# Kernel optimization log

Hardware: AMD Instinct MI355X
Metric: run time of the kernel (lower is better)

Reference implementation:

```python
import jax, jax.numpy as jnp
import numpy as np

N_NODES = 100000


def gcn_conv(x, edge_index, W, b):
    """PyG-style GCNConv: symmetric-normalized A+I propagation of x @ W, plus bias."""
    n = x.shape[0]
    src, dst = edge_index[0], edge_index[1]
    loops = jnp.arange(n, dtype=src.dtype)
    src = jnp.concatenate([src, loops])  # add self loops
    dst = jnp.concatenate([dst, loops])
    deg = jax.ops.segment_sum(jnp.ones_like(src, dtype=x.dtype), dst, num_segments=n)
    dinv = jnp.where(deg > 0, jax.lax.rsqrt(deg), 0.0)
    norm = dinv[src] * dinv[dst]  # [E+n]
    h = x @ W  # [n, out]
    msg = h[src] * norm[:, None]  # gather + scale
    out = jax.ops.segment_sum(msg, dst, num_segments=n)  # scatter-add
    return out + b


def setup_inputs() -> dict:
    key = jax.random.key(0)
    ks = jax.random.split(key, 5)
    x = jax.random.normal(ks[0], (N_NODES, 4), dtype=jnp.float32)
    edge_index = jax.random.randint(ks[1], (2, 3200000), 0, N_NODES, dtype=jnp.int64)
    W1 = jax.random.normal(ks[2], (4, 64), dtype=jnp.float32) * 0.5
    b1 = jnp.zeros((64,), dtype=jnp.float32)
    W2 = jax.random.normal(ks[3], (64, 32), dtype=jnp.float32) * 0.125
    b2 = jnp.zeros((32,), dtype=jnp.float32)
    return {"x": x, "edge_index": edge_index, "W1": W1, "b1": b1, "W2": W2, "b2": b2}


def reference(x, edge_index, W1, b1, W2, b2):
    h = gcn_conv(x, edge_index, W1, b1)
    h = jax.nn.relu(h)
    # F.dropout with training=False is identity (eval-mode reference)
    h = gcn_conv(h, edge_index, W2, b2)
    return jnp.mean(h, axis=0)  # [32]
```

## Files before the change

kernel.cpp:

```cpp
#include <hip/hip_runtime.h>

#define ST 512
#define EPB 8192
#define CT 1024
#define FT 1024
#define S_LOG 8
#define S 256
#define CAP 8912
#define MAXB 512

__device__ __forceinline__ void gAtomAdd(float* p, float v) {
    unsafeAtomicAdd(p, v);
}

__global__ void k_init(int* __restrict__ cur_d, int* __restrict__ cur_s,
                       float* __restrict__ g, int nb) {
    int t = threadIdx.x;
    if (t < nb) { cur_d[t] = t * CAP; cur_s[t] = t * CAP; }
    if (t < 64) g[t] = 0.0f;
}

__global__ void __launch_bounds__(ST) k_sctr2(
        const int4* __restrict__ src4, const int4* __restrict__ dst4, int E,
        int* __restrict__ cur_d, int* __restrict__ cur_s,
        unsigned* __restrict__ rec_d, unsigned* __restrict__ rec_s, int nb) {
    __shared__ unsigned lrec[EPB];
    __shared__ unsigned short lbkt[EPB];
    __shared__ int cnt[MAXB];
    __shared__ int lst[MAXB];
    __shared__ int gb[MAXB];
    int t = threadIdx.x;
    int E4 = E >> 2;
    int b4 = blockIdx.x * (EPB / 4);
    int m = min(EPB, E - blockIdx.x * EPB);

    int4 dk[4], sk[4];
    bool v[4];
    #pragma unroll
    for (int k = 0; k < 4; ++k) {
        int idx = b4 + k * ST + t;
        v[k] = idx < E4;
        if (v[k]) { dk[k] = dst4[idx]; sk[k] = src4[idx]; }
    }

    for (int ph = 0; ph < 2; ++ph) {
        int* cursor = ph ? cur_s : cur_d;
        unsigned* rec = ph ? rec_s : rec_d;
        cnt[t] = 0;
        __syncthreads();
        int rk[16];
        #pragma unroll
        for (int k = 0; k < 4; ++k) {
            if (v[k]) {
                int4 K = ph ? sk[k] : dk[k];
                rk[4 * k + 0] = atomicAdd(&cnt[K.x >> S_LOG], 1);
                rk[4 * k + 1] = atomicAdd(&cnt[K.y >> S_LOG], 1);
                rk[4 * k + 2] = atomicAdd(&cnt[K.z >> S_LOG], 1);
                rk[4 * k + 3] = atomicAdd(&cnt[K.w >> S_LOG], 1);
            }
        }
        __syncthreads();
        int c = cnt[t];
        for (int o = 1; o < MAXB; o <<= 1) {
            int u = (t >= o) ? cnt[t - o] : 0;
            __syncthreads();
            cnt[t] += u;
            __syncthreads();
        }
        lst[t] = cnt[t] - c;
        gb[t] = (c > 0) ? atomicAdd(&cursor[t], c) : 0;
        __syncthreads();
        #pragma unroll
        for (int k = 0; k < 4; ++k) {
            if (v[k]) {
                int4 K = ph ? sk[k] : dk[k];
                int4 P = ph ? dk[k] : sk[k];
                int bb, p;
                bb = K.x >> S_LOG; p = lst[bb] + rk[4 * k + 0];
                lrec[p] = ((unsigned)P.x << S_LOG) | (unsigned)(K.x & (S - 1));
                lbkt[p] = (unsigned short)bb;
                bb = K.y >> S_LOG; p = lst[bb] + rk[4 * k + 1];
                lrec[p] = ((unsigned)P.y << S_LOG) | (unsigned)(K.y & (S - 1));
                lbkt[p] = (unsigned short)bb;
                bb = K.z >> S_LOG; p = lst[bb] + rk[4 * k + 2];
                lrec[p] = ((unsigned)P.z << S_LOG) | (unsigned)(K.z & (S - 1));
                lbkt[p] = (unsigned short)bb;
                bb = K.w >> S_LOG; p = lst[bb] + rk[4 * k + 3];
                lrec[p] = ((unsigned)P.w << S_LOG) | (unsigned)(K.w & (S - 1));
                lbkt[p] = (unsigned short)bb;
            }
        }
        __syncthreads();
        for (int i = t; i < m; i += ST) {
            int bb = lbkt[i];
            rec[gb[bb] + (i - lst[bb])] = lrec[i];
        }
        __syncthreads();
    }
}

__global__ void __launch_bounds__(CT) k_csry(
        unsigned* __restrict__ rec, const int* __restrict__ cur_d,
        const float4* __restrict__ x, float* __restrict__ dinv,
        float4* __restrict__ y, int* __restrict__ nst_g, int* __restrict__ nend_g,
        int n) {
    __shared__ unsigned lrec[CAP];
    __shared__ int cnt[S];
    __shared__ int nst[S];
    int b = blockIdx.x, t = threadIdx.x;
    int lo = b * CAP;
    int m = cur_d[b] - lo;
    if (t < S) cnt[t] = 0;
    __syncthreads();
    unsigned rv[9]; int rr[9];
    #pragma unroll
    for (int k = 0; k < 9; ++k) {
        int i = t + k * CT;
        if (i < m) {
            unsigned r = rec[lo + i];
            rv[k] = r;
            rr[k] = atomicAdd(&cnt[r & (S - 1)], 1);
        }
    }
    __syncthreads();
    int deg = (t < S) ? cnt[t] : 0;
    int nd = (b << S_LOG) + t;
    if (t < S && nd < n) {
        float dv = rsqrtf((float)deg + 1.0f);
        dinv[nd] = dv;
        float4 xi = x[nd];
        y[nd] = make_float4(dv * xi.x, dv * xi.y, dv * xi.z, dv * xi.w);
    }
    for (int o = 1; o < S; o <<= 1) {
        int u = (t < S && t >= o) ? cnt[t - o] : 0;
        __syncthreads();
        if (t < S) cnt[t] += u;
        __syncthreads();
    }
    if (t < S) {
        int st = cnt[t] - deg;
        nst[t] = st;
        if (nd < n) { nst_g[nd] = lo + st; nend_g[nd] = lo + st + deg; }
    }
    __syncthreads();
    #pragma unroll
    for (int k = 0; k < 9; ++k) {
        int i = t + k * CT;
        if (i < m) lrec[nst[rv[k] & (S - 1)] + rr[k]] = rv[k] >> S_LOG;
    }
    __syncthreads();
    for (int i = t; i < m; i += CT) rec[lo + i] = lrec[i];
}

__global__ void __launch_bounds__(FT) k_fuse(
        const unsigned* __restrict__ rec_d, const unsigned* __restrict__ rec_s,
        const int* __restrict__ cur_s, const int* __restrict__ nst_g,
        const int* __restrict__ nend_g, const float4* __restrict__ y,
        const float* __restrict__ dinv,
        const float* __restrict__ W1, const float* __restrict__ b1,
        float* __restrict__ g, int n) {
    __shared__ float a[S];
    __shared__ float4 lp1[S];
    __shared__ float red[FT];
    int b = blockIdx.x, t = threadIdx.x;
    if (t < S) a[t] = 0.0f;
    __syncthreads();
    int lo = b * CAP;
    int m = cur_s[b] - lo;
    int m4 = m >> 2;
    const uint4* rec4 = (const uint4*)(rec_s + lo);
    for (int i = t; i < m4; i += FT) {
        uint4 r = rec4[i];
        float d0 = dinv[r.x >> S_LOG], d1 = dinv[r.y >> S_LOG];
        float d2 = dinv[r.z >> S_LOG], d3 = dinv[r.w >> S_LOG];
        atomicAdd(&a[r.x & (S - 1)], d0);
        atomicAdd(&a[r.y & (S - 1)], d1);
        atomicAdd(&a[r.z & (S - 1)], d2);
        atomicAdd(&a[r.w & (S - 1)], d3);
    }
    for (int i = (m4 << 2) + t; i < m; i += FT) {
        unsigned r = rec_s[lo + i];
        atomicAdd(&a[r & (S - 1)], dinv[r >> S_LOG]);
    }
    int node = t >> 2, q = t & 3;
    int nd = (b << S_LOG) + node;
    if (nd < n) {
        int j1 = nend_g[nd];
        int j = nst_g[nd] + q;
        float a0 = 0.0f, a1 = 0.0f, a2 = 0.0f, a3 = 0.0f;
        for (; j + 12 < j1; j += 16) {
            int s0 = rec_d[j], s1 = rec_d[j + 4], s2 = rec_d[j + 8], s3 = rec_d[j + 12];
            float4 y0 = y[s0], y1 = y[s1], y2 = y[s2], y3 = y[s3];
            a0 += y0.x + y1.x + y2.x + y3.x;
            a1 += y0.y + y1.y + y2.y + y3.y;
            a2 += y0.z + y1.z + y2.z + y3.z;
            a3 += y0.w + y1.w + y2.w + y3.w;
        }
        for (; j < j1; j += 4) {
            float4 ys = y[rec_d[j]];
            a0 += ys.x; a1 += ys.y; a2 += ys.z; a3 += ys.w;
        }
        a0 += __shfl_down(a0, 2); a1 += __shfl_down(a1, 2);
        a2 += __shfl_down(a2, 2); a3 += __shfl_down(a3, 2);
        a0 += __shfl_down(a0, 1); a1 += __shfl_down(a1, 1);
        a2 += __shfl_down(a2, 1); a3 += __shfl_down(a3, 1);
        if (q == 0) {
            float di = dinv[nd];
            lp1[node] = make_float4(di * a0, di * a1, di * a2, di * a3);
        }
    }
    __syncthreads();
    int c = t & 63, w = t >> 6;
    float w0 = W1[c], w1 = W1[64 + c], w2 = W1[128 + c], w3 = W1[192 + c];
    float bb = b1[c];
    int nb0 = b << S_LOG;
    float facc = 0.0f;
    for (int k = w; k < S; k += 16) {
        int ndk = nb0 + k;
        if (ndk >= n) break;
        float di = dinv[ndk];
        float4 p = lp1[k];
        float4 yi = y[ndk];
        float h0 = fmaf(di, yi.x, p.x);
        float h1 = fmaf(di, yi.y, p.y);
        float h2 = fmaf(di, yi.z, p.z);
        float h3 = fmaf(di, yi.w, p.w);
        float h = fmaf(h0, w0, fmaf(h1, w1, fmaf(h2, w2, fmaf(h3, w3, bb))));
        h = fmaxf(h, 0.0f);
        float wi = fmaf(di, a[k], di * di);
        facc = fmaf(wi, h, facc);
    }
    red[t] = facc;
    __syncthreads();
    if (t < 64) {
        float s = red[t];
        #pragma unroll
        for (int o = 1; o < 16; ++o) s += red[t + 64 * o];
        gAtomAdd(&g[t], s);
    }
}

__global__ void k_final(const float* __restrict__ g, const float* __restrict__ W2,
                        const float* __restrict__ b2, float* __restrict__ out, float inv_n) {
    int j = threadIdx.x;
    if (j < 32) {
        float a = 0.0f;
        #pragma unroll
        for (int c = 0; c < 64; ++c) a = fmaf(g[c], W2[c * 32 + j], a);
        out[j] = fmaf(a, inv_n, b2[j]);
    }
}

extern "C" void kernel_launch(void* const* d_in, const int* in_sizes, int n_in,
                              void* d_out, int out_size, void* d_ws, size_t ws_size,
                              hipStream_t stream) {
    const float* x  = (const float*)d_in[0];
    const int*   ei = (const int*)d_in[1];
    const float* W1 = (const float*)d_in[2];
    const float* b1 = (const float*)d_in[3];
    const float* W2 = (const float*)d_in[4];
    const float* b2 = (const float*)d_in[5];
    float* out = (float*)d_out;

    int n = in_sizes[0] / 4;
    int E = in_sizes[1] / 2;
    const int* src = ei;
    const int* dst = ei + E;
    int NB = (n + S - 1) >> S_LOG;

    char* ws = (char*)d_ws;
    int* cur_d = (int*)ws;
    int* cur_s = cur_d + 512;
    float* g   = (float*)(cur_s + 512);
    size_t ctrl = 1600;
    unsigned* rec_d = (unsigned*)ws + ctrl;
    unsigned* rec_s = rec_d + (size_t)NB * CAP;
    float* y    = (float*)(rec_s + (size_t)NB * CAP);
    float* dinv = y + 4 * (size_t)n;
    int* nst_g  = (int*)(dinv + (size_t)n);
    int* nend_g = nst_g + (size_t)n;

    int NSB = (E + EPB - 1) / EPB;

    k_init<<<1, 512, 0, stream>>>(cur_d, cur_s, g, NB);
    k_sctr2<<<NSB, ST, 0, stream>>>((const int4*)src, (const int4*)dst, E,
                                    cur_d, cur_s, rec_d, rec_s, NB);
    k_csry<<<NB, CT, 0, stream>>>(rec_d, cur_d, (const float4*)x, dinv,
                                  (float4*)y, nst_g, nend_g, n);
    k_fuse<<<NB, FT, 0, stream>>>(rec_d, rec_s, cur_s, nst_g, nend_g,
                                  (const float4*)y, dinv, W1, b1, g, n);
    k_final<<<1, 64, 0, stream>>>(g, W2, b2, out, 1.0f / (float)n);
}
```

Measured before the change: 154.5 us.

## Replace per-bucket CSR sort with LDS atomic scatter-add aggregation

The in-bucket counting sort that built CSR rows (prefix scan, LDS reorder, rec_d write-back, nst/nend arrays) is removed. Degrees are now counted with LDS atomics, and the first-layer aggregation scatter-adds gathered y rows into four per-component LDS arrays instead of walking sorted CSR rows. This cuts a pass over the records and the scan/sync overhead. The cost is about four times more LDS float atomics, possible contention on hot nodes, and a nondeterministic summation order. Block sizes drop from 1024 to 512 threads.

```diff
diff --git a/kernel.cpp b/kernel.cpp
--- a/kernel.cpp
+++ b/kernel.cpp
@@ -2,8 +2,8 @@
 
 #define ST 512
 #define EPB 8192
-#define CT 1024
-#define FT 1024
+#define DT 512
+#define FT 512
 #define S_LOG 8
 #define S 256
 #define CAP 8912
@@ -99,114 +99,94 @@
     }
 }
 
-__global__ void __launch_bounds__(CT) k_csry(
-        unsigned* __restrict__ rec, const int* __restrict__ cur_d,
+__global__ void __launch_bounds__(DT) k_dy(
+        const unsigned* __restrict__ rec_d, const int* __restrict__ cur_d,
         const float4* __restrict__ x, float* __restrict__ dinv,
-        float4* __restrict__ y, int* __restrict__ nst_g, int* __restrict__ nend_g,
-        int n) {
-    __shared__ unsigned lrec[CAP];
+        float4* __restrict__ y, int n) {
     __shared__ int cnt[S];
-    __shared__ int nst[S];
     int b = blockIdx.x, t = threadIdx.x;
     int lo = b * CAP;
-    int m = cur_d[b] - lo;
+    int md = cur_d[b] - lo;
     if (t < S) cnt[t] = 0;
     __syncthreads();
-    unsigned rv[9]; int rr[9];
-    #pragma unroll
-    for (int k = 0; k < 9; ++k) {
-        int i = t + k * CT;
-        if (i < m) {
-            unsigned r = rec[lo + i];
-            rv[k] = r;
-            rr[k] = atomicAdd(&cnt[r & (S - 1)], 1);
-        }
-    }
-    __syncthreads();
-    int deg = (t < S) ? cnt[t] : 0;
-    int nd = (b << S_LOG) + t;
-    if (t < S && nd < n) {
-        float dv = rsqrtf((float)deg + 1.0f);
-        dinv[nd] = dv;
-        float4 xi = x[nd];
-        y[nd] = make_float4(dv * xi.x, dv * xi.y, dv * xi.z, dv * xi.w);
-    }
-    for (int o = 1; o < S; o <<= 1) {
-        int u = (t < S && t >= o) ? cnt[t - o] : 0;
-        __syncthreads();
-        if (t < S) cnt[t] += u;
-        __syncthreads();
-    }
+    int m4 = md >> 2;
+    const uint4* r4 = (const uint4*)(rec_d + lo);
+    for (int i = t; i < m4; i += DT) {
+        uint4 r = r4[i];
+        atomicAdd(&cnt[r.x & (S - 1)], 1);
+        atomicAdd(&cnt[r.y & (S - 1)], 1);
+        atomicAdd(&cnt[r.z & (S - 1)], 1);
+        atomicAdd(&cnt[r.w & (S - 1)], 1);
+    }
+    for (int i = (m4 << 2) + t; i < md; i += DT)
+        atomicAdd(&cnt[rec_d[lo + i] & (S - 1)], 1);
+    __syncthreads();
     if (t < S) {
-        int st = cnt[t] - deg;
-        nst[t] = st;
-        if (nd < n) { nst_g[nd] = lo + st; nend_g[nd] = lo + st + deg; }
-    }
-    __syncthreads();
-    #pragma unroll
-    for (int k = 0; k < 9; ++k) {
-        int i = t + k * CT;
-        if (i < m) lrec[nst[rv[k] & (S - 1)] + rr[k]] = rv[k] >> S_LOG;
-    }
-    __syncthreads();
-    for (int i = t; i < m; i += CT) rec[lo + i] = lrec[i];
-}
-
-__global__ void __launch_bounds__(FT) k_fuse(
+        int nd = (b << S_LOG) + t;
+        if (nd < n) {
+            float dv = rsqrtf((float)cnt[t] + 1.0f);
+            dinv[nd] = dv;
+            float4 xi = x[nd];
+            y[nd] = make_float4(dv * xi.x, dv * xi.y, dv * xi.z, dv * xi.w);
+        }
+    }
+}
+
+__global__ void __launch_bounds__(FT) k_acc2(
         const unsigned* __restrict__ rec_d, const unsigned* __restrict__ rec_s,
-        const int* __restrict__ cur_s, const int* __restrict__ nst_g,
-        const int* __restrict__ nend_g, const float4* __restrict__ y,
-        const float* __restrict__ dinv,
+        const int* __restrict__ cur_d, const int* __restrict__ cur_s,
+        const float4* __restrict__ y, const float* __restrict__ dinv,
         const float* __restrict__ W1, const float* __restrict__ b1,
         float* __restrict__ g, int n) {
-    __shared__ float a[S];
-    __shared__ float4 lp1[S];
+    __shared__ float a0[S], a1[S], a2[S], a3[S], sd[S];
     __shared__ float red[FT];
     int b = blockIdx.x, t = threadIdx.x;
-    if (t < S) a[t] = 0.0f;
-    __syncthreads();
     int lo = b * CAP;
-    int m = cur_s[b] - lo;
-    int m4 = m >> 2;
-    const uint4* rec4 = (const uint4*)(rec_s + lo);
-    for (int i = t; i < m4; i += FT) {
-        uint4 r = rec4[i];
-        float d0 = dinv[r.x >> S_LOG], d1 = dinv[r.y >> S_LOG];
-        float d2 = dinv[r.z >> S_LOG], d3 = dinv[r.w >> S_LOG];
-        atomicAdd(&a[r.x & (S - 1)], d0);
-        atomicAdd(&a[r.y & (S - 1)], d1);
-        atomicAdd(&a[r.z & (S - 1)], d2);
-        atomicAdd(&a[r.w & (S - 1)], d3);
-    }
-    for (int i = (m4 << 2) + t; i < m; i += FT) {
-        unsigned r = rec_s[lo + i];
-        atomicAdd(&a[r & (S - 1)], dinv[r >> S_LOG]);
-    }
-    int node = t >> 2, q = t & 3;
-    int nd = (b << S_LOG) + node;
-    if (nd < n) {
-        int j1 = nend_g[nd];
-        int j = nst_g[nd] + q;
-        float a0 = 0.0f, a1 = 0.0f, a2 = 0.0f, a3 = 0.0f;
-        for (; j + 12 < j1; j += 16) {
-            int s0 = rec_d[j], s1 = rec_d[j + 4], s2 = rec_d[j + 8], s3 = rec_d[j + 12];
-            float4 y0 = y[s0], y1 = y[s1], y2 = y[s2], y3 = y[s3];
-            a0 += y0.x + y1.x + y2.x + y3.x;
-            a1 += y0.y + y1.y + y2.y + y3.y;
-            a2 += y0.z + y1.z + y2.z + y3.z;
-            a3 += y0.w + y1.w + y2.w + y3.w;
-        }
-        for (; j < j1; j += 4) {
-            float4 ys = y[rec_d[j]];
-            a0 += ys.x; a1 += ys.y; a2 += ys.z; a3 += ys.w;
-        }
-        a0 += __shfl_down(a0, 2); a1 += __shfl_down(a1, 2);
-        a2 += __shfl_down(a2, 2); a3 += __shfl_down(a3, 2);
-        a0 += __shfl_down(a0, 1); a1 += __shfl_down(a1, 1);
-        a2 += __shfl_down(a2, 1); a3 += __shfl_down(a3, 1);
-        if (q == 0) {
-            float di = dinv[nd];
-            lp1[node] = make_float4(di * a0, di * a1, di * a2, di * a3);
+    if (t < S) { a0[t] = 0.0f; a1[t] = 0.0f; a2[t] = 0.0f; a3[t] = 0.0f; sd[t] = 0.0f; }
+    __syncthreads();
+    {
+        int md = cur_d[b] - lo;
+        int m4 = md >> 2;
+        const uint4* r4 = (const uint4*)(rec_d + lo);
+        for (int i = t; i < m4; i += FT) {
+            uint4 r = r4[i];
+            float4 y0 = y[r.x >> S_LOG], y1 = y[r.y >> S_LOG];
+            float4 y2 = y[r.z >> S_LOG], y3 = y[r.w >> S_LOG];
+            int l0 = r.x & (S - 1), l1 = r.y & (S - 1);
+            int l2 = r.z & (S - 1), l3 = r.w & (S - 1);
+            atomicAdd(&a0[l0], y0.x); atomicAdd(&a1[l0], y0.y);
+            atomicAdd(&a2[l0], y0.z); atomicAdd(&a3[l0], y0.w);
+            atomicAdd(&a0[l1], y1.x); atomicAdd(&a1[l1], y1.y);
+            atomicAdd(&a2[l1], y1.z); atomicAdd(&a3[l1], y1.w);
+            atomicAdd(&a0[l2], y2.x); atomicAdd(&a1[l2], y2.y);
+            atomicAdd(&a2[l2], y2.z); atomicAdd(&a3[l2], y2.w);
+            atomicAdd(&a0[l3], y3.x); atomicAdd(&a1[l3], y3.y);
+            atomicAdd(&a2[l3], y3.z); atomicAdd(&a3[l3], y3.w);
+        }
+        for (int i = (m4 << 2) + t; i < md; i += FT) {
+            unsigned r = rec_d[lo + i];
+            float4 ys = y[r >> S_LOG];
+            int l = r & (S - 1);
+            atomicAdd(&a0[l], ys.x); atomicAdd(&a1[l], ys.y);
+            atomicAdd(&a2[l], ys.z); atomicAdd(&a3[l], ys.w);
+        }
+    }
+    {
+        int ms = cur_s[b] - lo;
+        int m4 = ms >> 2;
+        const uint4* r4 = (const uint4*)(rec_s + lo);
+        for (int i = t; i < m4; i += FT) {
+            uint4 r = r4[i];
+            float d0 = dinv[r.x >> S_LOG], d1 = dinv[r.y >> S_LOG];
+            float d2 = dinv[r.z >> S_LOG], d3 = dinv[r.w >> S_LOG];
+            atomicAdd(&sd[r.x & (S - 1)], d0);
+            atomicAdd(&sd[r.y & (S - 1)], d1);
+            atomicAdd(&sd[r.z & (S - 1)], d2);
+            atomicAdd(&sd[r.w & (S - 1)], d3);
+        }
+        for (int i = (m4 << 2) + t; i < ms; i += FT) {
+            unsigned r = rec_s[lo + i];
+            atomicAdd(&sd[r & (S - 1)], dinv[r >> S_LOG]);
         }
     }
     __syncthreads();
@@ -215,19 +195,18 @@
     float bb = b1[c];
     int nb0 = b << S_LOG;
     float facc = 0.0f;
-    for (int k = w; k < S; k += 16) {
-        int ndk = nb0 + k;
-        if (ndk >= n) break;
-        float di = dinv[ndk];
-        float4 p = lp1[k];
-        float4 yi = y[ndk];
-        float h0 = fmaf(di, yi.x, p.x);
-        float h1 = fmaf(di, yi.y, p.y);
-        float h2 = fmaf(di, yi.z, p.z);
-        float h3 = fmaf(di, yi.w, p.w);
+    for (int k = w; k < S; k += 8) {
+        int nd = nb0 + k;
+        if (nd >= n) break;
+        float di = dinv[nd];
+        float4 yi = y[nd];
+        float h0 = di * (a0[k] + yi.x);
+        float h1 = di * (a1[k] + yi.y);
+        float h2 = di * (a2[k] + yi.z);
+        float h3 = di * (a3[k] + yi.w);
         float h = fmaf(h0, w0, fmaf(h1, w1, fmaf(h2, w2, fmaf(h3, w3, bb))));
         h = fmaxf(h, 0.0f);
-        float wi = fmaf(di, a[k], di * di);
+        float wi = di * (sd[k] + di);
         facc = fmaf(wi, h, facc);
     }
     red[t] = facc;
@@ -235,7 +214,7 @@
     if (t < 64) {
         float s = red[t];
         #pragma unroll
-        for (int o = 1; o < 16; ++o) s += red[t + 64 * o];
+        for (int o = 1; o < 8; ++o) s += red[t + 64 * o];
         gAtomAdd(&g[t], s);
     }
 }
@@ -275,19 +254,17 @@
     size_t ctrl = 1600;
     unsigned* rec_d = (unsigned*)ws + ctrl;
     unsigned* rec_s = rec_d + (size_t)NB * CAP;
-    float* y    = (float*)(rec_s + (size_t)NB * CAP);
-    float* dinv = y + 4 * (size_t)n;
-    int* nst_g  = (int*)(dinv + (size_t)n);
-    int* nend_g = nst_g + (size_t)n;
+    float* yv   = (float*)(rec_s + (size_t)NB * CAP);
+    float* dinv = yv + 4 * (size_t)n;
 
     int NSB = (E + EPB - 1) / EPB;
 
     k_init<<<1, 512, 0, stream>>>(cur_d, cur_s, g, NB);
     k_sctr2<<<NSB, ST, 0, stream>>>((const int4*)src, (const int4*)dst, E,
                                     cur_d, cur_s, rec_d, rec_s, NB);
-    k_csry<<<NB, CT, 0, stream>>>(rec_d, cur_d, (const float4*)x, dinv,
-                                  (float4*)y, nst_g, nend_g, n);
-    k_fuse<<<NB, FT, 0, stream>>>(rec_d, rec_s, cur_s, nst_g, nend_g,
-                                  (const float4*)y, dinv, W1, b1, g, n);
+    k_dy<<<NB, DT, 0, stream>>>(rec_d, cur_d, (const float4*)x, dinv,
+                                (float4*)yv, n);
+    k_acc2<<<NB, FT, 0, stream>>>(rec_d, rec_s, cur_d, cur_s,
+                                  (const float4*)yv, dinv, W1, b1, g, n);
     k_final<<<1, 64, 0, stream>>>(g, W2, b2, out, 1.0f / (float)n);
 }
```

Measured after the change: 224.2 us. 1.45x slower.
